# Kernel tuning notes

Hardware: AMD Instinct MI355X
Metric: run time of the kernel (lower is better)

Reference implementation:

```python
import jax, jax.numpy as jnp
import numpy as np

CLAMP = 80.0


def setup_inputs() -> dict:
    key = jax.random.key(0)
    ks = jax.random.split(key, 8)
    B, C, D, H, W = 2, 64, 16, 16, 16
    Ck = C // 8  # qk channel dim
    x = jax.random.normal(ks[0], (B, C, D, H, W), dtype=jnp.float32)
    # 1x1x1 Conv3d == pointwise linear over channels
    wq = jax.random.normal(ks[1], (Ck, C), dtype=jnp.float32) * (1.0 / np.sqrt(C))
    bq = jnp.zeros((Ck,), dtype=jnp.float32)
    wk = jax.random.normal(ks[2], (Ck, C), dtype=jnp.float32) * (1.0 / np.sqrt(C))
    bk = jnp.zeros((Ck,), dtype=jnp.float32)
    wv = jax.random.normal(ks[3], (C, C), dtype=jnp.float32) * (1.0 / np.sqrt(C))
    bv = jnp.zeros((C,), dtype=jnp.float32)
    gamma = jnp.zeros((1,), dtype=jnp.float32)
    return {"x": x, "wq": wq, "bq": bq, "wk": wk, "bk": bk,
            "wv": wv, "bv": bv, "gamma": gamma}


def reference(x, wq, bq, wk, bk, wv, bv, gamma):
    B, C, D, H, W = x.shape
    N = D * H * W
    scale = 1.0 / np.sqrt(max(C // 8, 1))
    xf = x.reshape(B, C, N)
    # 1x1 convs as channel matmuls -> [B, Cq, N] / [B, C, N]
    q = jnp.einsum('oc,bcn->bon', wq, xf) + bq[None, :, None]
    k = jnp.einsum('oc,bcn->bon', wk, xf) + bk[None, :, None]
    v = jnp.einsum('oc,bcn->bon', wv, xf) + bv[None, :, None]
    q32, k32, v32 = q.astype(jnp.float32), k.astype(jnp.float32), v.astype(jnp.float32)
    # logits[b,n,m] = sum_o q[b,o,n] k[b,o,m] * scale  (q^T k)
    logits = jnp.einsum('bon,bom->bnm', q32, k32) * scale
    logits = jnp.clip(logits, -CLAMP, CLAMP)
    attn = jax.nn.softmax(logits, axis=-1)  # rows sum to 1
    # out = v @ attn  (note: attn applied on the right, as in source)
    out32 = jnp.einsum('bcn,bnm->bcm', v32, attn)
    out = out32.reshape(B, C, D, H, W).astype(x.dtype)
    return gamma[0] * out + x
```

## Files before the change

kernel.cpp:

```cpp
#include <hip/hip_runtime.h>

#define S2F (0.35355339059327373f * 1.4426950408889634f)

using h2 = decltype(__builtin_amdgcn_cvt_pkrtz(0.0f, 0.0f));
typedef _Float16 half8 __attribute__((ext_vector_type(8)));
typedef float f32x4 __attribute__((ext_vector_type(4)));

static __device__ __forceinline__ h2 u2h(unsigned u) { return __builtin_bit_cast(h2, u); }
static __device__ __forceinline__ unsigned pkf16(float a, float b) {
  return __builtin_bit_cast(unsigned, __builtin_amdgcn_cvt_pkrtz(a, b));
}
static __device__ __forceinline__ half8 u4h8(uint4 u) { return __builtin_bit_cast(half8, u); }


__global__ void __launch_bounds__(256, 4)
qkv_kernel(const float* __restrict__ x,
           const float* __restrict__ wq, const float* __restrict__ bq,
           const float* __restrict__ wk, const float* __restrict__ bk,
           const float* __restrict__ wv, const float* __restrict__ bv,
           unsigned* __restrict__ q4, unsigned* __restrict__ k4,
           unsigned* __restrict__ v16) {
  __shared__ float wls[16][64];
  __shared__ float bias16[16];
  __shared__ float qk_lds[16][32];
  int t = threadIdx.x;
  int bid = blockIdx.x;
  int b = bid / 640;
  int rem = bid - b * 640;
  int tile = rem / 5;
  int type = rem - tile * 5;
  int n0 = tile << 5;
  int j = t & 31, rg = t >> 5;

  float* wflat = &wls[0][0];
  for (int i = t; i < 1024; i += 256) {
    float wv_;
    if (type == 0) wv_ = (i < 512) ? wq[i] : wk[i - 512];
    else           wv_ = wv[((type - 1) << 10) + i];
    wflat[i] = wv_;
  }
  if (t < 16)
    bias16[t] = (type == 0) ? ((t < 8) ? bq[t] : bk[t - 8])
                            : bv[((type - 1) << 4) + t];
  __syncthreads();

  float res0 = bias16[rg * 2], res1 = bias16[rg * 2 + 1];
  const float* xb = x + ((b * 64) << 12) + n0 + j;
  #pragma unroll 1
  for (int c0 = 0; c0 < 64; c0 += 16) {
    float xr[16];
    #pragma unroll
    for (int cc = 0; cc < 16; ++cc) xr[cc] = xb[(c0 + cc) << 12];
    const float4* w0 = (const float4*)&wls[rg * 2][c0];
    const float4* w1 = (const float4*)&wls[rg * 2 + 1][c0];
    #pragma unroll
    for (int c4 = 0; c4 < 4; ++c4) {
      float4 a = w0[c4], bb = w1[c4];
      res0 += a.x * xr[4*c4] + a.y * xr[4*c4+1] + a.z * xr[4*c4+2] + a.w * xr[4*c4+3];
      res1 += bb.x * xr[4*c4] + bb.y * xr[4*c4+1] + bb.z * xr[4*c4+2] + bb.w * xr[4*c4+3];
    }
  }

  if (type == 0) {
    qk_lds[rg * 2][j] = res0;
    qk_lds[rg * 2 + 1][j] = res1;
    __syncthreads();
    if (t < 64) {
      int jj = t & 31;
      bool isq = t < 32;
      int rb = isq ? 0 : 8;
      float sc = isq ? S2F : 1.0f;
      uint4 u;
      u.x = pkf16(sc * qk_lds[rb + 0][jj], sc * qk_lds[rb + 1][jj]);
      u.y = pkf16(sc * qk_lds[rb + 2][jj], sc * qk_lds[rb + 3][jj]);
      u.z = pkf16(sc * qk_lds[rb + 4][jj], sc * qk_lds[rb + 5][jj]);
      u.w = pkf16(sc * qk_lds[rb + 6][jj], sc * qk_lds[rb + 7][jj]);
      unsigned* dst = isq ? q4 : k4;
      *(uint4*)&dst[((b << 12) + n0 + jj) << 2] = u;
    }
  } else {
    int cbase = (type - 1) << 4;
    unsigned nb0 = (unsigned)__builtin_amdgcn_ds_swizzle(
        __builtin_bit_cast(int, res0), 0x041F);
    unsigned nb1 = (unsigned)__builtin_amdgcn_ds_swizzle(
        __builtin_bit_cast(int, res1), 0x041F);
    if (!(j & 1)) {
      int u = j >> 1;
      int up = ((u & 6) << 1) | (((u >> 3) & 1) << 1) | (u & 1);
      int base = (((b << 7) + tile) << 10);
      v16[base + ((cbase + rg * 2) << 4) + up]     = pkf16(res0, __builtin_bit_cast(float, nb0));
      v16[base + ((cbase + rg * 2 + 1) << 4) + up] = pkf16(res1, __builtin_bit_cast(float, nb1));
    }
  }
}

__global__ void __launch_bounds__(512, 2)
rowsum_kernel(const unsigned* __restrict__ q4, const unsigned* __restrict__ k4,
              float* __restrict__ lsv2) {
  __shared__ float ps[8][16];
  int t = threadIdx.x;
  int b = blockIdx.x >> 8;
  int n0 = (blockIdx.x & 255) << 4;
  int w = t >> 6, l = t & 63;
  int L15 = l & 15, G = l >> 4;

  const unsigned* q4b = q4 + ((long)(b << 12) << 2);
  const unsigned* k4b = k4 + ((long)(b << 12) << 2);

  half8 aq0 = u4h8(*(const uint4*)&q4b[(n0 + L15) << 2]);

  f32x4 acc0 = {0.f, 0.f, 0.f, 0.f};
  #pragma unroll 8
  for (int s = 0; s < 32; ++s) {
    int m0 = (w << 9) + (s << 4);
    uint4 bku = (l < 16) ? *(const uint4*)&k4b[(m0 + L15) << 2]
                         : make_uint4(0, 0, 0, 0);
    half8 bk = u4h8(bku);
    f32x4 z = {0.f, 0.f, 0.f, 0.f};
    f32x4 d0 = __builtin_amdgcn_mfma_f32_16x16x32_f16(aq0, bk, z, 0, 0, 0);
    #pragma unroll
    for (int r = 0; r < 4; ++r) acc0[r] += exp2f(d0[r]);
  }
  #pragma unroll
  for (int r = 0; r < 4; ++r) {
    float a0 = acc0[r];
    a0 += __shfl_xor(a0, 1); a0 += __shfl_xor(a0, 2);
    a0 += __shfl_xor(a0, 4); a0 += __shfl_xor(a0, 8);
    acc0[r] = a0;
  }
  if (L15 == 0) {
    #pragma unroll
    for (int r = 0; r < 4; ++r) ps[w][(G << 2) + r] = acc0[r];
  }
  __syncthreads();
  if (t < 16) {
    float s = 0.f;
    #pragma unroll
    for (int ww = 0; ww < 8; ++ww) s += ps[ww][t];
    lsv2[(b << 12) + n0 + t] = -__log2f(s);
  }
}

__global__ void __launch_bounds__(512, 1)
attnout_kernel(const float* __restrict__ x, const unsigned* __restrict__ q4,
               const unsigned* __restrict__ k4, const unsigned* __restrict__ v16,
               const float* __restrict__ lsv2, const float* __restrict__ gamma,
               float* __restrict__ out) {
  __shared__ float red[8][64][36];
  int t = threadIdx.x;
  int b = blockIdx.x >> 7;
  int m0 = (blockIdx.x & 127) << 5;
  int w = t >> 6, l = t & 63;
  int L15 = l & 15, G = l >> 4;

  uint4 bk2[2];
  #pragma unroll
  for (int mh = 0; mh < 2; ++mh) {
    if (l < 16) bk2[mh] = *(const uint4*)&k4[((b << 12) + m0 + mh * 16 + L15) << 2];
    else        bk2[mh] = make_uint4(0, 0, 0, 0);
  }
  f32x4 acc[2][4];
  #pragma unroll
  for (int mh = 0; mh < 2; ++mh)
    #pragma unroll
    for (int cf = 0; cf < 4; ++cf) acc[mh][cf] = (f32x4){0.f, 0.f, 0.f, 0.f};

  const float* svb = lsv2 + (b << 12);
  const unsigned* q4b = q4 + ((long)(b << 12) << 2);
  const unsigned* v16b = v16 + ((long)b << 17);

  auto LOAD = [&](int step, half8& aq0, half8& aq1, f32x4& sv0, f32x4& sv1,
                  uint4* va) {
    int n0 = (w << 9) + (step << 5);
    int nblk = (w << 4) + step;
    aq0 = u4h8(*(const uint4*)&q4b[(n0 + L15) << 2]);
    aq1 = u4h8(*(const uint4*)&q4b[(n0 + 16 + L15) << 2]);
    sv0 = *(const f32x4*)&svb[n0 + (G << 2)];
    sv1 = *(const f32x4*)&svb[n0 + 16 + (G << 2)];
    const unsigned* vblk = v16b + (nblk << 10);
    #pragma unroll
    for (int cf = 0; cf < 4; ++cf)
      va[cf] = *(const uint4*)&vblk[(((cf << 4) + L15) << 4) + (G << 2)];
  };
  auto COMPUTE = [&](half8 aq0, half8 aq1, f32x4 sv0, f32x4 sv1, const uint4* va) {
    #pragma unroll
    for (int mh = 0; mh < 2; ++mh) {
      f32x4 z = {0.f, 0.f, 0.f, 0.f};
      f32x4 d0 = __builtin_amdgcn_mfma_f32_16x16x32_f16(aq0, u4h8(bk2[mh]), z, 0, 0, 0);
      f32x4 d1 = __builtin_amdgcn_mfma_f32_16x16x32_f16(aq1, u4h8(bk2[mh]), z, 0, 0, 0);
      float p0[4], p1[4];
      #pragma unroll
      for (int r = 0; r < 4; ++r) {
        p0[r] = exp2f(d0[r] + sv0[r]);
        p1[r] = exp2f(d1[r] + sv1[r]);
      }
      uint4 Bu;
      Bu.x = pkf16(p0[0], p0[1]);
      Bu.y = pkf16(p0[2], p0[3]);
      Bu.z = pkf16(p1[0], p1[1]);
      Bu.w = pkf16(p1[2], p1[3]);
      half8 Bf = u4h8(Bu);
      #pragma unroll
      for (int cf = 0; cf < 4; ++cf)
        acc[mh][cf] = __builtin_amdgcn_mfma_f32_16x16x32_f16(u4h8(va[cf]), Bf, acc[mh][cf], 0, 0, 0);
    }
  };

  half8 aq0A, aq1A, aq0B, aq1B;
  f32x4 sv0A, sv1A, sv0B, sv1B;
  uint4 vaA[4], vaB[4];
  LOAD(0, aq0A, aq1A, sv0A, sv1A, vaA);
  #pragma unroll 1
  for (int step = 0; step < 16; step += 2) {
    LOAD(step + 1, aq0B, aq1B, sv0B, sv1B, vaB);
    COMPUTE(aq0A, aq1A, sv0A, sv1A, vaA);
    if (step < 14) LOAD(step + 2, aq0A, aq1A, sv0A, sv1A, vaA);
    COMPUTE(aq0B, aq1B, sv0B, sv1B, vaB);
  }

  #pragma unroll
  for (int mh = 0; mh < 2; ++mh)
    #pragma unroll
    for (int cf = 0; cf < 4; ++cf)
      *(f32x4*)&red[w][l][(mh * 4 + cf) * 4] = acc[mh][cf];
  __syncthreads();
  int rl = t & 63, f = t >> 6;
  float g = gamma[0];
  f32x4 s = {0.f, 0.f, 0.f, 0.f};
  #pragma unroll
  for (int ww = 0; ww < 8; ++ww) s += *(const f32x4*)&red[ww][rl][f * 4];
  int mh = f >> 2, cf = f & 3;
  int m = m0 + mh * 16 + (rl & 15);
  int cb = cf * 16 + ((rl >> 4) << 2);
  #pragma unroll
  for (int r = 0; r < 4; ++r) {
    int idx = (((b << 6) + cb + r) << 12) + m;
    out[idx] = g * s[r] + x[idx];
  }
}

extern "C" void kernel_launch(void* const* d_in, const int* in_sizes, int n_in,
                              void* d_out, int out_size, void* d_ws, size_t ws_size,
                              hipStream_t stream) {
  const float* x     = (const float*)d_in[0];
  const float* wq    = (const float*)d_in[1];
  const float* bq    = (const float*)d_in[2];
  const float* wk    = (const float*)d_in[3];
  const float* bk    = (const float*)d_in[4];
  const float* wv    = (const float*)d_in[5];
  const float* bv    = (const float*)d_in[6];
  const float* gamma = (const float*)d_in[7];
  float* out = (float*)d_out;
  unsigned* wsu = (unsigned*)d_ws;
  unsigned* q4  = wsu;
  unsigned* k4  = wsu + 32768;
  unsigned* v16 = wsu + 65536;
  float*    lsv2 = (float*)(wsu + 327680);

  qkv_kernel<<<1280, 256, 0, stream>>>(x, wq, bq, wk, bk, wv, bv, q4, k4, v16);
  rowsum_kernel<<<512, 512, 0, stream>>>(q4, k4, lsv2);
  attnout_kernel<<<256, 512, 0, stream>>>(x, q4, k4, v16, lsv2, gamma, out);
}
```

Measured before the change: 40.43 us.

## Split QK projection from V projection and co-schedule V with rowsum

```diff
diff --git a/kernel.cpp b/kernel.cpp
--- a/kernel.cpp
+++ b/kernel.cpp
@@ -14,34 +14,23 @@
 
 
 __global__ void __launch_bounds__(256, 4)
-qkv_kernel(const float* __restrict__ x,
-           const float* __restrict__ wq, const float* __restrict__ bq,
-           const float* __restrict__ wk, const float* __restrict__ bk,
-           const float* __restrict__ wv, const float* __restrict__ bv,
-           unsigned* __restrict__ q4, unsigned* __restrict__ k4,
-           unsigned* __restrict__ v16) {
+qk_kernel(const float* __restrict__ x,
+          const float* __restrict__ wq, const float* __restrict__ bq,
+          const float* __restrict__ wk, const float* __restrict__ bk,
+          unsigned* __restrict__ q4, unsigned* __restrict__ k4) {
   __shared__ float wls[16][64];
   __shared__ float bias16[16];
   __shared__ float qk_lds[16][32];
   int t = threadIdx.x;
   int bid = blockIdx.x;
-  int b = bid / 640;
-  int rem = bid - b * 640;
-  int tile = rem / 5;
-  int type = rem - tile * 5;
-  int n0 = tile << 5;
+  int b = bid >> 7;
+  int n0 = (bid & 127) << 5;
   int j = t & 31, rg = t >> 5;
 
   float* wflat = &wls[0][0];
-  for (int i = t; i < 1024; i += 256) {
-    float wv_;
-    if (type == 0) wv_ = (i < 512) ? wq[i] : wk[i - 512];
-    else           wv_ = wv[((type - 1) << 10) + i];
-    wflat[i] = wv_;
-  }
-  if (t < 16)
-    bias16[t] = (type == 0) ? ((t < 8) ? bq[t] : bk[t - 8])
-                            : bv[((type - 1) << 4) + t];
+  for (int i = t; i < 1024; i += 256)
+    wflat[i] = (i < 512) ? wq[i] : wk[i - 512];
+  if (t < 16) bias16[t] = (t < 8) ? bq[t] : bk[t - 8];
   __syncthreads();
 
   float res0 = bias16[rg * 2], res1 = bias16[rg * 2 + 1];
@@ -61,25 +50,104 @@
     }
   }
 
-  if (type == 0) {
-    qk_lds[rg * 2][j] = res0;
-    qk_lds[rg * 2 + 1][j] = res1;
+  qk_lds[rg * 2][j] = res0;
+  qk_lds[rg * 2 + 1][j] = res1;
+  __syncthreads();
+  if (t < 64) {
+    int jj = t & 31;
+    bool isq = t < 32;
+    int rb = isq ? 0 : 8;
+    float sc = isq ? S2F : 1.0f;
+    uint4 u;
+    u.x = pkf16(sc * qk_lds[rb + 0][jj], sc * qk_lds[rb + 1][jj]);
+    u.y = pkf16(sc * qk_lds[rb + 2][jj], sc * qk_lds[rb + 3][jj]);
+    u.z = pkf16(sc * qk_lds[rb + 4][jj], sc * qk_lds[rb + 5][jj]);
+    u.w = pkf16(sc * qk_lds[rb + 6][jj], sc * qk_lds[rb + 7][jj]);
+    unsigned* dst = isq ? q4 : k4;
+    *(uint4*)&dst[((b << 12) + n0 + jj) << 2] = u;
+  }
+}
+
+__global__ void __launch_bounds__(256, 4)
+rsvp_kernel(const float* __restrict__ x,
+            const float* __restrict__ wv, const float* __restrict__ bv,
+            const unsigned* __restrict__ q4, const unsigned* __restrict__ k4,
+            unsigned* __restrict__ v16, float* __restrict__ lsv2) {
+  __shared__ float sh[1040];
+  int t = threadIdx.x;
+  int bid = blockIdx.x;
+
+  if (bid < 512) {
+    float* ps = sh;
+    int b = bid >> 8;
+    int n0 = (bid & 255) << 4;
+    int w = t >> 6, l = t & 63;
+    int L15 = l & 15, G = l >> 4;
+    const unsigned* q4b = q4 + ((long)(b << 12) << 2);
+    const unsigned* k4b = k4 + ((long)(b << 12) << 2);
+    half8 aq0 = u4h8(*(const uint4*)&q4b[(n0 + L15) << 2]);
+    f32x4 acc0 = {0.f, 0.f, 0.f, 0.f};
+    #pragma unroll 8
+    for (int s = 0; s < 64; ++s) {
+      int m0 = (w << 10) + (s << 4);
+      uint4 bku = (l < 16) ? *(const uint4*)&k4b[(m0 + L15) << 2]
+                           : make_uint4(0, 0, 0, 0);
+      f32x4 z = {0.f, 0.f, 0.f, 0.f};
+      f32x4 d0 = __builtin_amdgcn_mfma_f32_16x16x32_f16(aq0, u4h8(bku), z, 0, 0, 0);
+      #pragma unroll
+      for (int r = 0; r < 4; ++r) acc0[r] += exp2f(d0[r]);
+    }
+    #pragma unroll
+    for (int r = 0; r < 4; ++r) {
+      float a0 = acc0[r];
+      a0 += __shfl_xor(a0, 1); a0 += __shfl_xor(a0, 2);
+      a0 += __shfl_xor(a0, 4); a0 += __shfl_xor(a0, 8);
+      acc0[r] = a0;
+    }
+    if (L15 == 0) {
+      #pragma unroll
+      for (int r = 0; r < 4; ++r) ps[w * 16 + (G << 2) + r] = acc0[r];
+    }
     __syncthreads();
-    if (t < 64) {
-      int jj = t & 31;
-      bool isq = t < 32;
-      int rb = isq ? 0 : 8;
-      float sc = isq ? S2F : 1.0f;
-      uint4 u;
-      u.x = pkf16(sc * qk_lds[rb + 0][jj], sc * qk_lds[rb + 1][jj]);
-      u.y = pkf16(sc * qk_lds[rb + 2][jj], sc * qk_lds[rb + 3][jj]);
-      u.z = pkf16(sc * qk_lds[rb + 4][jj], sc * qk_lds[rb + 5][jj]);
-      u.w = pkf16(sc * qk_lds[rb + 6][jj], sc * qk_lds[rb + 7][jj]);
-      unsigned* dst = isq ? q4 : k4;
-      *(uint4*)&dst[((b << 12) + n0 + jj) << 2] = u;
+    if (t < 16) {
+      float s = 0.f;
+      #pragma unroll
+      for (int ww = 0; ww < 4; ++ww) s += ps[ww * 16 + t];
+      lsv2[(b << 12) + n0 + t] = -__log2f(s);
     }
   } else {
-    int cbase = (type - 1) << 4;
+    float* wls = sh;
+    float* bias16 = sh + 1024;
+    int idx = bid - 512;
+    int b = idx >> 9;
+    int rem = idx & 511;
+    int tile = rem >> 2;
+    int cg = rem & 3;
+    int n0 = tile << 5;
+    int j = t & 31, rg = t >> 5;
+
+    for (int i = t; i < 1024; i += 256) wls[i] = wv[(cg << 10) + i];
+    if (t < 16) bias16[t] = bv[(cg << 4) + t];
+    __syncthreads();
+
+    float res0 = bias16[rg * 2], res1 = bias16[rg * 2 + 1];
+    const float* xb = x + ((b * 64) << 12) + n0 + j;
+    #pragma unroll 1
+    for (int c0 = 0; c0 < 64; c0 += 16) {
+      float xr[16];
+      #pragma unroll
+      for (int cc = 0; cc < 16; ++cc) xr[cc] = xb[(c0 + cc) << 12];
+      const float4* w0 = (const float4*)&wls[(rg * 2) * 64 + c0];
+      const float4* w1 = (const float4*)&wls[(rg * 2 + 1) * 64 + c0];
+      #pragma unroll
+      for (int c4 = 0; c4 < 4; ++c4) {
+        float4 a = w0[c4], bb = w1[c4];
+        res0 += a.x * xr[4*c4] + a.y * xr[4*c4+1] + a.z * xr[4*c4+2] + a.w * xr[4*c4+3];
+        res1 += bb.x * xr[4*c4] + bb.y * xr[4*c4+1] + bb.z * xr[4*c4+2] + bb.w * xr[4*c4+3];
+      }
+    }
+
+    int cbase = cg << 4;
     unsigned nb0 = (unsigned)__builtin_amdgcn_ds_swizzle(
         __builtin_bit_cast(int, res0), 0x041F);
     unsigned nb1 = (unsigned)__builtin_amdgcn_ds_swizzle(
@@ -91,53 +159,6 @@
       v16[base + ((cbase + rg * 2) << 4) + up]     = pkf16(res0, __builtin_bit_cast(float, nb0));
       v16[base + ((cbase + rg * 2 + 1) << 4) + up] = pkf16(res1, __builtin_bit_cast(float, nb1));
     }
-  }
-}
-
-__global__ void __launch_bounds__(512, 2)
-rowsum_kernel(const unsigned* __restrict__ q4, const unsigned* __restrict__ k4,
-              float* __restrict__ lsv2) {
-  __shared__ float ps[8][16];
-  int t = threadIdx.x;
-  int b = blockIdx.x >> 8;
-  int n0 = (blockIdx.x & 255) << 4;
-  int w = t >> 6, l = t & 63;
-  int L15 = l & 15, G = l >> 4;
-
-  const unsigned* q4b = q4 + ((long)(b << 12) << 2);
-  const unsigned* k4b = k4 + ((long)(b << 12) << 2);
-
-  half8 aq0 = u4h8(*(const uint4*)&q4b[(n0 + L15) << 2]);
-
-  f32x4 acc0 = {0.f, 0.f, 0.f, 0.f};
-  #pragma unroll 8
-  for (int s = 0; s < 32; ++s) {
-    int m0 = (w << 9) + (s << 4);
-    uint4 bku = (l < 16) ? *(const uint4*)&k4b[(m0 + L15) << 2]
-                         : make_uint4(0, 0, 0, 0);
-    half8 bk = u4h8(bku);
-    f32x4 z = {0.f, 0.f, 0.f, 0.f};
-    f32x4 d0 = __builtin_amdgcn_mfma_f32_16x16x32_f16(aq0, bk, z, 0, 0, 0);
-    #pragma unroll
-    for (int r = 0; r < 4; ++r) acc0[r] += exp2f(d0[r]);
-  }
-  #pragma unroll
-  for (int r = 0; r < 4; ++r) {
-    float a0 = acc0[r];
-    a0 += __shfl_xor(a0, 1); a0 += __shfl_xor(a0, 2);
-    a0 += __shfl_xor(a0, 4); a0 += __shfl_xor(a0, 8);
-    acc0[r] = a0;
-  }
-  if (L15 == 0) {
-    #pragma unroll
-    for (int r = 0; r < 4; ++r) ps[w][(G << 2) + r] = acc0[r];
-  }
-  __syncthreads();
-  if (t < 16) {
-    float s = 0.f;
-    #pragma unroll
-    for (int ww = 0; ww < 8; ++ww) s += ps[ww][t];
-    lsv2[(b << 12) + n0 + t] = -__log2f(s);
   }
 }
 
@@ -257,7 +278,7 @@
   unsigned* v16 = wsu + 65536;
   float*    lsv2 = (float*)(wsu + 327680);
 
-  qkv_kernel<<<1280, 256, 0, stream>>>(x, wq, bq, wk, bk, wv, bv, q4, k4, v16);
-  rowsum_kernel<<<512, 512, 0, stream>>>(q4, k4, lsv2);
+  qk_kernel<<<256, 256, 0, stream>>>(x, wq, bq, wk, bk, q4, k4);
+  rsvp_kernel<<<1536, 256, 0, stream>>>(x, wv, bv, q4, k4, v16, lsv2);
   attnout_kernel<<<256, 512, 0, stream>>>(x, q4, k4, v16, lsv2, gamma, out);
 }
```

Result: slower. 46.57 us (+15.2%).
